# Performance work log

Hardware: AMD Instinct MI355X
Metric: run time of the kernel (lower is better)

## Reference

```python
import jax, jax.numpy as jnp
import numpy as np

N_NODES = 10000
N_EDGES = 160000
FEAT = 32
EMB = 32
VOCAB = 32000
EDGE_DIM = 9
HID = 32  # edge MLP hidden


def setup_inputs() -> dict:
    key = jax.random.key(0)
    ks = jax.random.split(key, 16)
    s = lambda *sh: 1.0 / np.sqrt(sh[0])
    inp = {
        "signal": jax.random.randint(ks[0], (1,), 0, VOCAB, dtype=jnp.int64) if jax.config.jax_enable_x64 else jax.random.randint(ks[0], (1,), 0, VOCAB).astype(jnp.int32),
        "x": jax.random.normal(ks[1], (N_NODES, FEAT), dtype=jnp.float32),
        "edge_index": jax.random.randint(ks[2], (2, N_EDGES), 0, N_NODES).astype(jnp.int32),
        "edge_attr": jax.random.normal(ks[3], (N_EDGES, EDGE_DIM), dtype=jnp.float32),
        # edge MLP 1: 9 -> 32 -> FEAT*EMB
        "w1a": jax.random.normal(ks[4], (EDGE_DIM, HID), dtype=jnp.float32) * s(EDGE_DIM),
        "b1a": jnp.zeros((HID,), jnp.float32),
        "w1b": jax.random.normal(ks[5], (HID, FEAT * EMB), dtype=jnp.float32) * s(HID),
        "b1b": jnp.zeros((FEAT * EMB,), jnp.float32),
        "root1": jax.random.normal(ks[6], (FEAT, EMB), dtype=jnp.float32) * s(FEAT),
        "bias1": jnp.zeros((EMB,), jnp.float32),
        # edge MLP 2: 9 -> 32 -> EMB*EMB
        "w2a": jax.random.normal(ks[7], (EDGE_DIM, HID), dtype=jnp.float32) * s(EDGE_DIM),
        "b2a": jnp.zeros((HID,), jnp.float32),
        "w2b": jax.random.normal(ks[8], (HID, EMB * EMB), dtype=jnp.float32) * s(HID),
        "b2b": jnp.zeros((EMB * EMB,), jnp.float32),
        "root2": jax.random.normal(ks[9], (EMB, EMB), dtype=jnp.float32) * s(EMB),
        "bias2": jnp.zeros((EMB,), jnp.float32),
        "emb_table": jax.random.normal(ks[10], (VOCAB, EMB), dtype=jnp.float32),
    }
    return inp


def nnconv(x, edge_index, edge_attr, wa, ba, wb, bb, root, bias, in_ch, out_ch):
    # edge MLP -> per-edge weight matrices [E, in_ch, out_ch]
    h = jax.nn.relu(edge_attr @ wa + ba)
    W_e = (h @ wb + bb).reshape(-1, in_ch, out_ch)
    src, dst = edge_index[0], edge_index[1]
    # gather source node features, per-edge matmul
    msg = jnp.einsum("ei,eio->eo", x[src], W_e)  # [E, out_ch]
    summed = jax.ops.segment_sum(msg, dst, num_segments=N_NODES)
    cnt = jax.ops.segment_sum(jnp.ones((msg.shape[0],), msg.dtype), dst, num_segments=N_NODES)
    aggr = summed / jnp.maximum(cnt, 1.0)[:, None]  # scatter-mean (0 for isolated nodes)
    return aggr + x @ root + bias


def reference(signal, x, edge_index, edge_attr,
              w1a, b1a, w1b, b1b, root1, bias1,
              w2a, b2a, w2b, b2b, root2, bias2, emb_table):
    h = jax.nn.relu(nnconv(x, edge_index, edge_attr, w1a, b1a, w1b, b1b, root1, bias1, FEAT, EMB))
    h = jax.nn.relu(nnconv(h, edge_index, edge_attr, w2a, b2a, w2b, b2b, root2, bias2, EMB, EMB))
    sig = emb_table[signal]          # [1, EMB]
    sig = sig[0]                      # squeeze leading 1 (matches torch branch)
    scores = h @ sig                  # [N]
    return jax.nn.log_softmax(scores, axis=0)
```

## Files before the change

kernel.cpp:

```cpp
#include <hip/hip_runtime.h>
#include <math.h>

#define NN 10000
#define NE 160000
#define C  32
#define ED 9
#define EAP 12

typedef __attribute__((ext_vector_type(8))) short short8v;
typedef __attribute__((ext_vector_type(4))) float float4v;

__device__ inline unsigned short f2bf(float f) {
    unsigned int u = __float_as_uint(f);
    return (unsigned short)((u + 0x7fffu + ((u >> 16) & 1u)) >> 16);
}
__device__ inline float bf2f(unsigned int us) { return __uint_as_float(us << 16); }

#define ZQ 10016
__global__ __launch_bounds__(256) void prep_kernel(uint4* __restrict__ zreg,
                                                   const float* __restrict__ w1b,
                                                   const float* __restrict__ w2b,
                                                   unsigned short* __restrict__ wbB1,
                                                   unsigned short* __restrict__ wbB2) {
    const int b = blockIdx.x, tid = threadIdx.x;
    if (b < 40) {
        const int i = b * 256 + tid;
        if (i < ZQ) zreg[i] = uint4{0u, 0u, 0u, 0u};
    } else if (b < 168) {
        const int idx = (b - 40) * 256 + tid;
        const int i = idx & 31, j = idx >> 5;
        wbB1[idx] = f2bf(w1b[(j & 31) * (C * C) + i * C + (j >> 5)]);
    } else {
        const int idx = (b - 168) * 256 + tid;
        const int i = idx & 31, j = idx >> 5;
        wbB2[idx] = f2bf(w2b[(j & 31) * (C * C) + i * C + (j >> 5)]);
    }
}

__global__ __launch_bounds__(256) void hist_kernel(const int* __restrict__ ei,
                                                   int* __restrict__ cnt_src,
                                                   int* __restrict__ cnt_dst) {
    const int e = blockIdx.x * 256 + threadIdx.x;
    if (e < NE) {
        atomicAdd(&cnt_src[ei[e]], 1);
        atomicAdd(&cnt_dst[ei[NE + e]], 1);
    }
}

__global__ __launch_bounds__(1024) void scan2_kernel(const int* __restrict__ cnt_src,
                                                     const int* __restrict__ cnt_dst,
                                                     int* __restrict__ offs,
                                                     int* __restrict__ doffs) {
    const int* cnt = blockIdx.x ? cnt_dst : cnt_src;
    int* out       = blockIdx.x ? doffs   : offs;
    __shared__ int wtot[16];
    const int t = threadIdx.x;
    const int lane = t & 63, wid = t >> 6;
    const int base = t * 10;
    int loc[10];
    int s = 0;
#pragma unroll
    for (int j = 0; j < 10; ++j) {
        int v = (base + j < NN) ? cnt[base + j] : 0;
        loc[j] = s;
        s += v;
    }
    int inc = s;
    for (int d = 1; d < 64; d <<= 1) {
        int v = __shfl_up(inc, d, 64);
        if (lane >= d) inc += v;
    }
    if (lane == 63) wtot[wid] = inc;
    __syncthreads();
    if (t < 16) {
        int w = wtot[t];
        for (int d = 1; d < 16; d <<= 1) {
            int v = __shfl_up(w, d, 64);
            if (t >= d) w += v;
        }
        wtot[t] = w;
    }
    __syncthreads();
    const int excl = inc - s + (wid ? wtot[wid - 1] : 0);
#pragma unroll
    for (int j = 0; j < 10; ++j)
        if (base + j < NN) out[base + j] = excl + loc[j];
    if (t == 1023) out[NN] = wtot[15];
}

__device__ __forceinline__ void u_mfma_body(int vb, int tid,
                                            float* __restrict__ xs,
                                            unsigned int* __restrict__ bhi,
                                            unsigned int* __restrict__ blo,
                                            const float* __restrict__ xin,
                                            const unsigned short* __restrict__ wbB,
                                            const float* __restrict__ bb,
                                            unsigned short* __restrict__ UT,
                                            float* __restrict__ xb) {
    const int nb = vb * 16;
    {
        const float2 v = *reinterpret_cast<const float2*>(xin + nb * C + 2 * tid);
        xs[2 * tid] = v.x; xs[2 * tid + 1] = v.y;
        const unsigned hx = f2bf(v.x), hy = f2bf(v.y);
        bhi[tid] = hx | (hy << 16);
        const float lx = v.x - bf2f(hx), ly = v.y - bf2f(hy);
        blo[tid] = (unsigned)f2bf(lx) | ((unsigned)f2bf(ly) << 16);
    }
    __syncthreads();

    const int w = tid >> 6, l = tid & 63;
    const int r15 = l & 15, q = l >> 4;
    const short8v Bh = *reinterpret_cast<const short8v*>(
        reinterpret_cast<const unsigned short*>(bhi) + r15 * C + q * 8);
    const short8v Bl = *reinterpret_cast<const short8v*>(
        reinterpret_cast<const unsigned short*>(blo) + r15 * C + q * 8);
    const float4v Z = {0.f, 0.f, 0.f, 0.f};

#pragma unroll
    for (int cg = 0; cg < 4; ++cg) {
        const int jbase = w * 256 + cg * 64 + 0;
#pragma unroll
        for (int t4 = 0; t4 < 4; ++t4) {
            const int jb = jbase + t4 * 16;
            const short8v A = *reinterpret_cast<const short8v*>(
                wbB + (size_t)(jb + r15) * C + q * 8);
            float4v acc = __builtin_amdgcn_mfma_f32_16x16x32_bf16(A, Bl, Z, 0, 0, 0);
            acc = __builtin_amdgcn_mfma_f32_16x16x32_bf16(A, Bh, acc, 0, 0, 0);
            ushort4 pk;
            pk.x = f2bf(acc[0]); pk.y = f2bf(acc[1]);
            pk.z = f2bf(acc[2]); pk.w = f2bf(acc[3]);
            *reinterpret_cast<ushort4*>(UT + (size_t)(nb + r15) * (C * C) + jb + q * 4) = pk;
        }
    }
#pragma unroll
    for (int t = 0; t < 2; ++t) {
        const int idx = t * 256 + tid;
        const int n = idx >> 5, oo = idx & 31;
        float acc = 0.f;
#pragma unroll
        for (int i = 0; i < C; ++i) acc += xs[n * C + i] * bb[i * C + oo];
        xb[(size_t)(nb + n) * C + oo] = acc;
    }
}

__global__ __launch_bounds__(256) void mid_kernel(const int* __restrict__ ei,
                                                  const float* __restrict__ ea,
                                                  const int* __restrict__ offs,
                                                  const int* __restrict__ doffs,
                                                  int* __restrict__ cur_src,
                                                  int* __restrict__ cur_dst,
                                                  int* __restrict__ pd,
                                                  float* __restrict__ ea_s,
                                                  const float* __restrict__ xin,
                                                  const unsigned short* __restrict__ wbB,
                                                  const float* __restrict__ bb,
                                                  unsigned short* __restrict__ UT,
                                                  float* __restrict__ xb) {
    __shared__ float xs[16 * C];
    __shared__ unsigned int bhi[256], blo[256];
    const int b = blockIdx.x, tid = threadIdx.x;
    if (b < 625) {
        const int e = b * 256 + tid;
        if (e < NE) {
            const int sn  = ei[e];
            const int dn  = ei[NE + e];
            const int pos = offs[sn]  + atomicAdd(&cur_src[sn], 1);
            const int dpo = doffs[dn] + atomicAdd(&cur_dst[dn], 1);
            pd[pos] = dpo;
#pragma unroll
            for (int j = 0; j < ED; ++j)
                ea_s[(size_t)pos * EAP + j] = ea[(size_t)e * ED + j];
        }
    } else {
        u_mfma_body(b - 625, tid, xs, bhi, blo, xin, wbB, bb, UT, xb);
    }
}

__global__ __launch_bounds__(256) void u_mfma(const float* __restrict__ xin,
                                              const unsigned short* __restrict__ wbB,
                                              const float* __restrict__ bb,
                                              unsigned short* __restrict__ UT,
                                              float* __restrict__ xb) {
    __shared__ float xs[16 * C];
    __shared__ unsigned int bhi[256], blo[256];
    u_mfma_body(blockIdx.x, threadIdx.x, xs, bhi, blo, xin, wbB, bb, UT, xb);
}

__global__ __launch_bounds__(256) void edge5_kernel(const int* __restrict__ offs,
                                                    const int* __restrict__ pd,
                                                    const float* __restrict__ ea_s,
                                                    const float* __restrict__ wa,
                                                    const float* __restrict__ ba,
                                                    const unsigned short* __restrict__ UT,
                                                    const float* __restrict__ xb,
                                                    float* __restrict__ msg) {
    __shared__ float was[ED * C];
    __shared__ float bas[C];
    const int tid = threadIdx.x;
    for (int t = tid; t < ED * C; t += 256) was[t] = wa[t];
    if (tid < C) bas[tid] = ba[tid];
    __syncthreads();

    const int w  = tid >> 6;
    const int l  = tid & 63;
    const int s  = blockIdx.x * 4 + w;
    const int q  = l >> 4;
    const int el = l & 15;

    const int e0 = offs[s], e1 = offs[s + 1];
    if (e0 == e1) return;

    const unsigned short* up = UT + (size_t)s * (C * C);
    const short8v B1 = *reinterpret_cast<const short8v*>(up + el * C + q * 8);
    const short8v B2 = *reinterpret_cast<const short8v*>(up + (el + 16) * C + q * 8);
    const float c1 = xb[s * C + el];
    const float c2 = xb[s * C + el + 16];
    const float4v C1 = {c1, c1, c1, c1};
    const float4v C2 = {c2, c2, c2, c2};
    float hb[8];
#pragma unroll
    for (int i = 0; i < 8; ++i) hb[i] = bas[q * 8 + i];

    for (int pb = e0; pb < e1; pb += 16) {
        const int p  = pb + el;
        const int pc = (p < e1) ? p : e0;
        const float* eap = ea_s + (size_t)pc * EAP;
        const float4v ea0 = *reinterpret_cast<const float4v*>(eap);
        const float4v ea1 = *reinterpret_cast<const float4v*>(eap + 4);
        const float   ea8 = eap[8];

        float h[8];
#pragma unroll
        for (int i = 0; i < 8; ++i) h[i] = hb[i];
#pragma unroll
        for (int j = 0; j < ED; ++j) {
            const float ev = (j == 0) ? ea0.x : (j == 1) ? ea0.y : (j == 2) ? ea0.z
                           : (j == 3) ? ea0.w : (j == 4) ? ea1.x : (j == 5) ? ea1.y
                           : (j == 6) ? ea1.z : (j == 7) ? ea1.w : ea8;
            const float4v w0 = *reinterpret_cast<const float4v*>(&was[j * C + q * 8]);
            const float4v w1 = *reinterpret_cast<const float4v*>(&was[j * C + q * 8 + 4]);
            h[0] += ev * w0.x; h[1] += ev * w0.y; h[2] += ev * w0.z; h[3] += ev * w0.w;
            h[4] += ev * w1.x; h[5] += ev * w1.y; h[6] += ev * w1.z; h[7] += ev * w1.w;
        }
        union { int u[4]; short8v v; } A;
#pragma unroll
        for (int v = 0; v < 4; ++v) {
            const unsigned lo = f2bf(fmaxf(h[2 * v], 0.f));
            const unsigned hi = f2bf(fmaxf(h[2 * v + 1], 0.f));
            A.u[v] = (int)(lo | (hi << 16));
        }
        const float4v d1 = __builtin_amdgcn_mfma_f32_16x16x32_bf16(A.v, B1, C1, 0, 0, 0);
        const float4v d2 = __builtin_amdgcn_mfma_f32_16x16x32_bf16(A.v, B2, C2, 0, 0, 0);
#pragma unroll
        for (int r = 0; r < 4; ++r) {
            const int pe = pb + q * 4 + r;
            if (pe < e1) {
                const int mr = pd[pe];
                msg[(size_t)mr * C + el]      = d1[r];
                msg[(size_t)mr * C + el + 16] = d2[r];
            }
        }
    }
}

__global__ __launch_bounds__(256) void nodeagg1_kernel(const int* __restrict__ doffs,
                                                       const float* __restrict__ msg,
                                                       const float* __restrict__ xin,
                                                       const float* __restrict__ root,
                                                       const float* __restrict__ bias,
                                                       float* __restrict__ h1out) {
    __shared__ float rs[C * C];
    __shared__ float bs[C];
    __shared__ float xls[4][C];
    const int tid = threadIdx.x;
    for (int t = tid; t < C * C; t += 256) rs[t] = root[t];
    if (tid < C) bs[tid] = bias[tid];
    __syncthreads();

    const int w = tid >> 6, lane = tid & 63;
    const int half = lane >> 5, o = lane & 31;
    const int d = blockIdx.x * 4 + w;
    const int e0 = doffs[d], e1 = doffs[d + 1];

    float acc = 0.f;
    for (int p = e0 + half; p < e1; p += 2) acc += msg[(size_t)p * C + o];
    acc += __shfl_down(acc, 32, 64);
    if (lane < 32) xls[w][o] = xin[(size_t)d * C + o];
    if (lane < 32) {
        const float cn = fmaxf((float)(e1 - e0), 1.f);
        float a = bs[o] + acc / cn;
#pragma unroll
        for (int i = 0; i < C; ++i) a += xls[w][i] * rs[i * C + o];
        h1out[(size_t)d * C + o] = fmaxf(a, 0.f);
    }
}

__global__ __launch_bounds__(256) void nodeagg2_score(const int* __restrict__ doffs,
                                                      const float* __restrict__ msg,
                                                      const float* __restrict__ h1,
                                                      const float* __restrict__ root,
                                                      const float* __restrict__ bias,
                                                      const float* __restrict__ emb,
                                                      const int* __restrict__ signal,
                                                      float* __restrict__ scores) {
    __shared__ float rs[C * C];
    __shared__ float bs[C];
    __shared__ float sig[C];
    __shared__ float xls[4][C];
    const int tid = threadIdx.x;
    for (int t = tid; t < C * C; t += 256) rs[t] = root[t];
    if (tid < C) {
        bs[tid]  = bias[tid];
        sig[tid] = emb[(size_t)signal[0] * C + tid];
    }
    __syncthreads();

    const int w = tid >> 6, lane = tid & 63;
    const int half = lane >> 5, o = lane & 31;
    const int d = blockIdx.x * 4 + w;
    const int e0 = doffs[d], e1 = doffs[d + 1];

    float acc = 0.f;
    for (int p = e0 + half; p < e1; p += 2) acc += msg[(size_t)p * C + o];
    acc += __shfl_down(acc, 32, 64);
    if (lane < 32) xls[w][o] = h1[(size_t)d * C + o];
    if (lane < 32) {
        const float cn = fmaxf((float)(e1 - e0), 1.f);
        float a = bs[o] + acc / cn;
#pragma unroll
        for (int i = 0; i < C; ++i) a += xls[w][i] * rs[i * C + o];
        float val = fmaxf(a, 0.f) * sig[o];
#pragma unroll
        for (int off = 16; off; off >>= 1) val += __shfl_xor(val, off, 32);
        if (o == 0) scores[d] = val;
    }
}

__global__ __launch_bounds__(1024) void reduce_out_kernel(const float* __restrict__ scores,
                                                          float* __restrict__ out) {
    __shared__ float sm[16];
    __shared__ float ss[16];
    const int tid = threadIdx.x;
    float m = -INFINITY;
    for (int n = tid; n < NN; n += 1024) m = fmaxf(m, scores[n]);
    for (int off = 32; off; off >>= 1) m = fmaxf(m, __shfl_down(m, off, 64));
    if ((tid & 63) == 0) sm[tid >> 6] = m;
    __syncthreads();
    if (tid == 0) {
        float mm = sm[0];
        for (int w = 1; w < 16; ++w) mm = fmaxf(mm, sm[w]);
        sm[0] = mm;
    }
    __syncthreads();
    const float gmax = sm[0];
    float s = 0.f;
    for (int n = tid; n < NN; n += 1024) s += expf(scores[n] - gmax);
    for (int off = 32; off; off >>= 1) s += __shfl_down(s, off, 64);
    if ((tid & 63) == 0) ss[tid >> 6] = s;
    __syncthreads();
    if (tid == 0) {
        float t = 0.f;
        for (int w = 0; w < 16; ++w) t += ss[w];
        ss[0] = logf(t);
    }
    __syncthreads();
    const float sub = gmax + ss[0];
    for (int n = tid; n < NN; n += 1024) out[n] = scores[n] - sub;
}

extern "C" void kernel_launch(void* const* d_in, const int* in_sizes, int n_in,
                              void* d_out, int out_size, void* d_ws, size_t ws_size,
                              hipStream_t stream) {
    const int*   signal = (const int*)d_in[0];
    const float* x      = (const float*)d_in[1];
    const int*   ei     = (const int*)d_in[2];
    const float* ea     = (const float*)d_in[3];
    const float* w1a    = (const float*)d_in[4];
    const float* b1a    = (const float*)d_in[5];
    const float* w1b    = (const float*)d_in[6];
    const float* b1b    = (const float*)d_in[7];
    const float* root1  = (const float*)d_in[8];
    const float* bias1  = (const float*)d_in[9];
    const float* w2a    = (const float*)d_in[10];
    const float* b2a    = (const float*)d_in[11];
    const float* w2b    = (const float*)d_in[12];
    const float* b2b    = (const float*)d_in[13];
    const float* root2  = (const float*)d_in[14];
    const float* bias2  = (const float*)d_in[15];
    const float* emb    = (const float*)d_in[16];

    float* ws = (float*)d_ws;
    unsigned short* UT = (unsigned short*)ws;
    float* msg     = ws + 5120000;
    float* xb      = msg + 5120000;
    float* h1      = xb + 320000;
    float* ea_s    = h1 + 320000;
    unsigned short* wbB1 = (unsigned short*)(ea_s + 1920000);
    unsigned short* wbB2 = wbB1 + 32768;
    float* scores  = ea_s + 1920000 + 32768;
    int*   offs    = (int*)(scores + 10000);
    int*   doffs   = offs + 10016;
    int*   pd      = doffs + 10016;
    int*   cnt_src = pd + 160000;
    int*   cnt_dst = cnt_src + NN;
    int*   cur_src = cnt_dst + NN;
    int*   cur_dst = cur_src + NN;

    prep_kernel<<<296, 256, 0, stream>>>((uint4*)cnt_src, w1b, w2b, wbB1, wbB2);
    hist_kernel<<<(NE + 255) / 256, 256, 0, stream>>>(ei, cnt_src, cnt_dst);
    scan2_kernel<<<2, 1024, 0, stream>>>(cnt_src, cnt_dst, offs, doffs);
    mid_kernel<<<1250, 256, 0, stream>>>(ei, ea, offs, doffs, cur_src, cur_dst,
                                         pd, ea_s, x, wbB1, b1b, UT, xb);
    edge5_kernel<<<2500, 256, 0, stream>>>(offs, pd, ea_s, w1a, b1a, UT, xb, msg);
    nodeagg1_kernel<<<2500, 256, 0, stream>>>(doffs, msg, x, root1, bias1, h1);
    u_mfma<<<625, 256, 0, stream>>>(h1, wbB2, b2b, UT, xb);
    edge5_kernel<<<2500, 256, 0, stream>>>(offs, pd, ea_s, w2a, b2a, UT, xb, msg);
    nodeagg2_score<<<2500, 256, 0, stream>>>(doffs, msg, h1, root2, bias2,
                                             emb, signal, scores);
    reduce_out_kernel<<<1, 1024, 0, stream>>>(scores, (float*)d_out);
}
```

Before: 143.8 us.

## Fuse histogram+scan into shared-memory setup kernel and nodeagg1 with layer-2 MFMA

Histogram, scan and weight prep now run in one setup kernel: each of two 1024-thread blocks builds its degree histogram with shared-memory atomics and scans it in place, so the separate global-atomic histogram pass and two launches go away. The layer-1 node aggregation is fused with the layer-2 per-node MFMA transform, so each block computes 16 h1 rows into LDS and feeds them straight into the MFMA, saving one launch and a reread of h1. The cost is that the whole 160k-edge histogram is handled by only two blocks, which serialises that stage, and the fused kernel runs 625 blocks instead of 2500.

```diff
diff --git a/kernel.cpp b/kernel.cpp
--- a/kernel.cpp
+++ b/kernel.cpp
@@ -16,94 +16,82 @@
 }
 __device__ inline float bf2f(unsigned int us) { return __uint_as_float(us << 16); }
 
-#define ZQ 10016
-__global__ __launch_bounds__(256) void prep_kernel(uint4* __restrict__ zreg,
-                                                   const float* __restrict__ w1b,
-                                                   const float* __restrict__ w2b,
-                                                   unsigned short* __restrict__ wbB1,
-                                                   unsigned short* __restrict__ wbB2) {
-    const int b = blockIdx.x, tid = threadIdx.x;
-    if (b < 40) {
-        const int i = b * 256 + tid;
-        if (i < ZQ) zreg[i] = uint4{0u, 0u, 0u, 0u};
-    } else if (b < 168) {
-        const int idx = (b - 40) * 256 + tid;
+__global__ __launch_bounds__(1024) void setup_kernel(const int* __restrict__ ei,
+                                                     int* __restrict__ offs,
+                                                     int* __restrict__ doffs,
+                                                     const float* __restrict__ w1b,
+                                                     const float* __restrict__ w2b,
+                                                     unsigned short* __restrict__ wbB1,
+                                                     unsigned short* __restrict__ wbB2,
+                                                     uint4* __restrict__ zcur) {
+    __shared__ int cnt[NN];
+    __shared__ int wtot[16];
+    const int b = blockIdx.x, t = threadIdx.x;
+    if (b < 2) {
+        for (int i = t; i < NN; i += 1024) cnt[i] = 0;
+        __syncthreads();
+        const int* col = ei + (b ? NE : 0);
+        for (int e = t; e < NE; e += 1024) atomicAdd(&cnt[col[e]], 1);
+        __syncthreads();
+        int* out = b ? doffs : offs;
+        const int lane = t & 63, wid = t >> 6;
+        const int base = t * 10;
+        int loc[10];
+        int s = 0;
+#pragma unroll
+        for (int j = 0; j < 10; ++j) {
+            int v = (base + j < NN) ? cnt[base + j] : 0;
+            loc[j] = s;
+            s += v;
+        }
+        int inc = s;
+        for (int d = 1; d < 64; d <<= 1) {
+            int v = __shfl_up(inc, d, 64);
+            if (lane >= d) inc += v;
+        }
+        if (lane == 63) wtot[wid] = inc;
+        __syncthreads();
+        if (t < 16) {
+            int w = wtot[t];
+            for (int d = 1; d < 16; d <<= 1) {
+                int v = __shfl_up(w, d, 64);
+                if (t >= d) w += v;
+            }
+            wtot[t] = w;
+        }
+        __syncthreads();
+        const int excl = inc - s + (wid ? wtot[wid - 1] : 0);
+#pragma unroll
+        for (int j = 0; j < 10; ++j)
+            if (base + j < NN) out[base + j] = excl + loc[j];
+        if (t == 1023) out[NN] = wtot[15];
+    } else if (b < 34) {
+        const int idx = (b - 2) * 1024 + t;
         const int i = idx & 31, j = idx >> 5;
         wbB1[idx] = f2bf(w1b[(j & 31) * (C * C) + i * C + (j >> 5)]);
-    } else {
-        const int idx = (b - 168) * 256 + tid;
+    } else if (b < 66) {
+        const int idx = (b - 34) * 1024 + t;
         const int i = idx & 31, j = idx >> 5;
         wbB2[idx] = f2bf(w2b[(j & 31) * (C * C) + i * C + (j >> 5)]);
-    }
-}
-
-__global__ __launch_bounds__(256) void hist_kernel(const int* __restrict__ ei,
-                                                   int* __restrict__ cnt_src,
-                                                   int* __restrict__ cnt_dst) {
-    const int e = blockIdx.x * 256 + threadIdx.x;
-    if (e < NE) {
-        atomicAdd(&cnt_src[ei[e]], 1);
-        atomicAdd(&cnt_dst[ei[NE + e]], 1);
-    }
-}
-
-__global__ __launch_bounds__(1024) void scan2_kernel(const int* __restrict__ cnt_src,
-                                                     const int* __restrict__ cnt_dst,
-                                                     int* __restrict__ offs,
-                                                     int* __restrict__ doffs) {
-    const int* cnt = blockIdx.x ? cnt_dst : cnt_src;
-    int* out       = blockIdx.x ? doffs   : offs;
-    __shared__ int wtot[16];
-    const int t = threadIdx.x;
-    const int lane = t & 63, wid = t >> 6;
-    const int base = t * 10;
-    int loc[10];
-    int s = 0;
-#pragma unroll
-    for (int j = 0; j < 10; ++j) {
-        int v = (base + j < NN) ? cnt[base + j] : 0;
-        loc[j] = s;
-        s += v;
-    }
-    int inc = s;
-    for (int d = 1; d < 64; d <<= 1) {
-        int v = __shfl_up(inc, d, 64);
-        if (lane >= d) inc += v;
-    }
-    if (lane == 63) wtot[wid] = inc;
-    __syncthreads();
-    if (t < 16) {
-        int w = wtot[t];
-        for (int d = 1; d < 16; d <<= 1) {
-            int v = __shfl_up(w, d, 64);
-            if (t >= d) w += v;
-        }
-        wtot[t] = w;
-    }
-    __syncthreads();
-    const int excl = inc - s + (wid ? wtot[wid - 1] : 0);
-#pragma unroll
-    for (int j = 0; j < 10; ++j)
-        if (base + j < NN) out[base + j] = excl + loc[j];
-    if (t == 1023) out[NN] = wtot[15];
-}
-
-__device__ __forceinline__ void u_mfma_body(int vb, int tid,
-                                            float* __restrict__ xs,
+    } else {
+        const int i = (b - 66) * 1024 + t;
+        if (i < 5016) zcur[i] = uint4{0u, 0u, 0u, 0u};
+    }
+}
+
+__device__ __forceinline__ void u_mfma_core(int nb, int tid,
+                                            const float* __restrict__ xs,
                                             unsigned int* __restrict__ bhi,
                                             unsigned int* __restrict__ blo,
-                                            const float* __restrict__ xin,
                                             const unsigned short* __restrict__ wbB,
                                             const float* __restrict__ bb,
                                             unsigned short* __restrict__ UT,
                                             float* __restrict__ xb) {
-    const int nb = vb * 16;
     {
-        const float2 v = *reinterpret_cast<const float2*>(xin + nb * C + 2 * tid);
-        xs[2 * tid] = v.x; xs[2 * tid + 1] = v.y;
-        const unsigned hx = f2bf(v.x), hy = f2bf(v.y);
+        const float vx = xs[2 * tid], vy = xs[2 * tid + 1];
+        const unsigned hx = f2bf(vx), hy = f2bf(vy);
         bhi[tid] = hx | (hy << 16);
-        const float lx = v.x - bf2f(hx), ly = v.y - bf2f(hy);
+        const float lx = vx - bf2f(hx), ly = vy - bf2f(hy);
         blo[tid] = (unsigned)f2bf(lx) | ((unsigned)f2bf(ly) << 16);
     }
     __syncthreads();
@@ -118,7 +106,7 @@
 
 #pragma unroll
     for (int cg = 0; cg < 4; ++cg) {
-        const int jbase = w * 256 + cg * 64 + 0;
+        const int jbase = w * 256 + cg * 64;
 #pragma unroll
         for (int t4 = 0; t4 < 4; ++t4) {
             const int jb = jbase + t4 * 16;
@@ -172,18 +160,12 @@
                 ea_s[(size_t)pos * EAP + j] = ea[(size_t)e * ED + j];
         }
     } else {
-        u_mfma_body(b - 625, tid, xs, bhi, blo, xin, wbB, bb, UT, xb);
-    }
-}
-
-__global__ __launch_bounds__(256) void u_mfma(const float* __restrict__ xin,
-                                              const unsigned short* __restrict__ wbB,
-                                              const float* __restrict__ bb,
-                                              unsigned short* __restrict__ UT,
-                                              float* __restrict__ xb) {
-    __shared__ float xs[16 * C];
-    __shared__ unsigned int bhi[256], blo[256];
-    u_mfma_body(blockIdx.x, threadIdx.x, xs, bhi, blo, xin, wbB, bb, UT, xb);
+        const int nb = (b - 625) * 16;
+        const float2 v = *reinterpret_cast<const float2*>(xin + nb * C + 2 * tid);
+        xs[2 * tid] = v.x; xs[2 * tid + 1] = v.y;
+        __syncthreads();
+        u_mfma_core(nb, tid, xs, bhi, blo, wbB, bb, UT, xb);
+    }
 }
 
 __global__ __launch_bounds__(256) void edge5_kernel(const int* __restrict__ offs,
@@ -263,36 +245,50 @@
     }
 }
 
-__global__ __launch_bounds__(256) void nodeagg1_kernel(const int* __restrict__ doffs,
-                                                       const float* __restrict__ msg,
-                                                       const float* __restrict__ xin,
-                                                       const float* __restrict__ root,
-                                                       const float* __restrict__ bias,
-                                                       float* __restrict__ h1out) {
+__global__ __launch_bounds__(256) void naggu_kernel(const int* __restrict__ doffs,
+                                                    const float* __restrict__ msg,
+                                                    const float* __restrict__ xin,
+                                                    const float* __restrict__ root1,
+                                                    const float* __restrict__ bias1,
+                                                    const unsigned short* __restrict__ wbB2,
+                                                    const float* __restrict__ b2b,
+                                                    unsigned short* __restrict__ UT,
+                                                    float* __restrict__ xb,
+                                                    float* __restrict__ h1out) {
     __shared__ float rs[C * C];
     __shared__ float bs[C];
+    __shared__ float xs[16 * C];
     __shared__ float xls[4][C];
+    __shared__ unsigned int bhi[256], blo[256];
     const int tid = threadIdx.x;
-    for (int t = tid; t < C * C; t += 256) rs[t] = root[t];
-    if (tid < C) bs[tid] = bias[tid];
+    for (int t = tid; t < C * C; t += 256) rs[t] = root1[t];
+    if (tid < C) bs[tid] = bias1[tid];
     __syncthreads();
 
     const int w = tid >> 6, lane = tid & 63;
     const int half = lane >> 5, o = lane & 31;
-    const int d = blockIdx.x * 4 + w;
-    const int e0 = doffs[d], e1 = doffs[d + 1];
-
-    float acc = 0.f;
-    for (int p = e0 + half; p < e1; p += 2) acc += msg[(size_t)p * C + o];
-    acc += __shfl_down(acc, 32, 64);
-    if (lane < 32) xls[w][o] = xin[(size_t)d * C + o];
-    if (lane < 32) {
-        const float cn = fmaxf((float)(e1 - e0), 1.f);
-        float a = bs[o] + acc / cn;
-#pragma unroll
-        for (int i = 0; i < C; ++i) a += xls[w][i] * rs[i * C + o];
-        h1out[(size_t)d * C + o] = fmaxf(a, 0.f);
-    }
+    const int nb = blockIdx.x * 16;
+
+    for (int r = 0; r < 4; ++r) {
+        const int d = nb + w * 4 + r;
+        const int e0 = doffs[d], e1 = doffs[d + 1];
+        float acc = 0.f;
+        for (int p = e0 + half; p < e1; p += 2) acc += msg[(size_t)p * C + o];
+        acc += __shfl_down(acc, 32, 64);
+        if (lane < 32) xls[w][o] = xin[(size_t)d * C + o];
+        if (lane < 32) {
+            const float cn = fmaxf((float)(e1 - e0), 1.f);
+            float a = bs[o] + acc / cn;
+#pragma unroll
+            for (int i = 0; i < C; ++i) a += xls[w][i] * rs[i * C + o];
+            const float hv = fmaxf(a, 0.f);
+            xs[(w * 4 + r) * C + o] = hv;
+            h1out[(size_t)d * C + o] = hv;
+        }
+    }
+    __syncthreads();
+
+    u_mfma_core(nb, tid, xs, bhi, blo, wbB2, b2b, UT, xb);
 }
 
 __global__ __launch_bounds__(256) void nodeagg2_score(const int* __restrict__ doffs,
@@ -392,28 +388,25 @@
     float* ws = (float*)d_ws;
     unsigned short* UT = (unsigned short*)ws;
     float* msg     = ws + 5120000;
-    float* xb      = msg + 5120000;
-    float* h1      = xb + 320000;
-    float* ea_s    = h1 + 320000;
-    unsigned short* wbB1 = (unsigned short*)(ea_s + 1920000);
-    unsigned short* wbB2 = wbB1 + 32768;
-    float* scores  = ea_s + 1920000 + 32768;
-    int*   offs    = (int*)(scores + 10000);
-    int*   doffs   = offs + 10016;
-    int*   pd      = doffs + 10016;
-    int*   cnt_src = pd + 160000;
-    int*   cnt_dst = cnt_src + NN;
-    int*   cur_src = cnt_dst + NN;
+    float* xb      = ws + 10240000;
+    float* h1      = ws + 10560000;
+    float* ea_s    = ws + 10880000;
+    unsigned short* wbB1 = (unsigned short*)(ws + 12800000);
+    unsigned short* wbB2 = (unsigned short*)(ws + 12816384);
+    float* scores  = ws + 12832768;
+    int*   offs    = (int*)(ws + 12842768);
+    int*   doffs   = (int*)(ws + 12852784);
+    int*   pd      = (int*)(ws + 12862800);
+    int*   cur_src = (int*)(ws + 13022800);
     int*   cur_dst = cur_src + NN;
 
-    prep_kernel<<<296, 256, 0, stream>>>((uint4*)cnt_src, w1b, w2b, wbB1, wbB2);
-    hist_kernel<<<(NE + 255) / 256, 256, 0, stream>>>(ei, cnt_src, cnt_dst);
-    scan2_kernel<<<2, 1024, 0, stream>>>(cnt_src, cnt_dst, offs, doffs);
+    setup_kernel<<<71, 1024, 0, stream>>>(ei, offs, doffs, w1b, w2b, wbB1, wbB2,
+                                          (uint4*)cur_src);
     mid_kernel<<<1250, 256, 0, stream>>>(ei, ea, offs, doffs, cur_src, cur_dst,
                                          pd, ea_s, x, wbB1, b1b, UT, xb);
     edge5_kernel<<<2500, 256, 0, stream>>>(offs, pd, ea_s, w1a, b1a, UT, xb, msg);
-    nodeagg1_kernel<<<2500, 256, 0, stream>>>(doffs, msg, x, root1, bias1, h1);
-    u_mfma<<<625, 256, 0, stream>>>(h1, wbB2, b2b, UT, xb);
+    naggu_kernel<<<625, 256, 0, stream>>>(doffs, msg, x, root1, bias1,
+                                          wbB2, b2b, UT, xb, h1);
     edge5_kernel<<<2500, 256, 0, stream>>>(offs, pd, ea_s, w2a, b2a, UT, xb, msg);
     nodeagg2_score<<<2500, 256, 0, stream>>>(doffs, msg, h1, root2, bias2,
                                              emb, signal, scores);
```

After: 161.0 us. 11.9% more time.
